# Kernel optimization log

Measured on AMD Instinct MI355X. Metric: run time of the kernel, lower is better.

Reference implementation:

```python
import jax, jax.numpy as jnp
import numpy as np

N_STREAMS = 4
TAU = 1.0
ALPHA = 0.1
CAYLEY_ITERS = 2
LN_EPS = 1e-5


def setup_inputs() -> dict:
    key = jax.random.key(0)
    k1, k2, k3 = jax.random.split(key, 3)
    b, l, d = 2, 4096, 2048
    n = N_STREAMS
    x = jax.random.normal(k1, (b, l, d), dtype=jnp.float32)
    ln_w = jnp.ones((d,), dtype=jnp.float32)
    ln_b = jnp.zeros((d,), dtype=jnp.float32)
    # CastedLinear: trunc_normal std = 1/sqrt(in_features)
    proj_w = jax.random.truncated_normal(k2, -2.0, 2.0, (3 * n * n, d), dtype=jnp.float32) / jnp.sqrt(d * 1.0)
    proj_b = jnp.zeros((3 * n * n,), dtype=jnp.float32)
    # sublayer_fn realized as a dense linear (typical transformer sublayer core)
    W_sub = jax.random.normal(k3, (d, d), dtype=jnp.float32) / jnp.sqrt(d * 1.0)
    return {"x": x, "ln_w": ln_w, "ln_b": ln_b, "proj_w": proj_w, "proj_b": proj_b, "W_sub": W_sub}


def _layernorm(x, w, b):
    mu = jnp.mean(x, axis=-1, keepdims=True)
    var = jnp.mean(jnp.square(x - mu), axis=-1, keepdims=True)
    return (x - mu) * jax.lax.rsqrt(var + LN_EPS) * w + b


def _iterative_cayley(raw):
    # raw: (b, l, n, n) fp32
    w = raw - jnp.swapaxes(raw, -1, -2)
    eye = jnp.eye(N_STREAMS, dtype=raw.dtype)
    y = eye + ALPHA * w
    for _ in range(CAYLEY_ITERS):
        y = eye + 0.5 * ALPHA * jnp.matmul(w, eye + y)
    return y


def reference(x, ln_w, ln_b, proj_w, proj_b, W_sub):
    b, l, d = x.shape
    n = N_STREAMS
    gates = _layernorm(x, ln_w, ln_b) @ proj_w.T + proj_b  # (b, l, 3*n*n)
    pre_raw, post_raw, res_raw = jnp.split(gates, 3, axis=-1)
    pre_raw = pre_raw.reshape(b, l, n, n).astype(jnp.float32)
    post_raw = post_raw.reshape(b, l, n, n).astype(jnp.float32)
    res_raw = res_raw.reshape(b, l, n, n).astype(jnp.float32)
    h_pre = jax.nn.softmax(pre_raw / TAU, axis=-1)
    h_post = jax.nn.softmax(post_raw / TAU, axis=-2)
    h_res = _iterative_cayley(res_raw)
    # All streams of x_streams are identical copies of x, so
    # einsum('blij,bljd->blid', h, x_streams).mean(-2) == mean_i(sum_j h[i,j]) * x.
    coeff_pre = jnp.mean(jnp.sum(h_pre, axis=-1), axis=-1)    # (b, l)
    coeff_res = jnp.mean(jnp.sum(h_res, axis=-1), axis=-1)    # (b, l)
    coeff_post = jnp.mean(jnp.sum(h_post, axis=-1), axis=-1)  # (b, l)
    x_in = coeff_pre[..., None] * x
    y = x_in @ W_sub  # sublayer_fn
    return coeff_res[..., None] * x + coeff_post[..., None] * y
```

## Files before the change

### kernel.cpp

```cpp
#include <hip/hip_runtime.h>
#include <stdint.h>


typedef __attribute__((ext_vector_type(8))) __bf16 bf16x8;
typedef __attribute__((ext_vector_type(4))) float f32x4;
typedef __attribute__((ext_vector_type(8))) unsigned short us8;
typedef __attribute__((ext_vector_type(4))) unsigned short us4;

__device__ __forceinline__ unsigned short f2bf(float f) {
  union { float f; unsigned int u; } v; v.f = f;
  unsigned int u = v.u;
  u += 0x7fffu + ((u >> 16) & 1u);
  return (unsigned short)(u >> 16);
}

__device__ __forceinline__ void gload_lds16(const void* g, void* l) {
  __builtin_amdgcn_global_load_lds(
      (__attribute__((address_space(1))) void*)g,
      (__attribute__((address_space(3))) void*)l, 16, 0, 0);
}

__global__ __launch_bounds__(256) void k_ln_conv(
    const float* __restrict__ x, const float* __restrict__ lw, const float* __restrict__ lb,
    unsigned short* __restrict__ xb, unsigned short* __restrict__ lnb, int D) {
  const int t = blockIdx.x;
  const int tid = threadIdx.x;
  const float* row = x + (size_t)t * D;
  f32x4 a = *(const f32x4*)(row + tid * 8);
  f32x4 b = *(const f32x4*)(row + tid * 8 + 4);
  float vv[8] = {a[0], a[1], a[2], a[3], b[0], b[1], b[2], b[3]};
  float s = 0.f, ss = 0.f;
#pragma unroll
  for (int j = 0; j < 8; ++j) { s += vv[j]; ss += vv[j] * vv[j]; }
#pragma unroll
  for (int off = 32; off > 0; off >>= 1) { s += __shfl_down(s, off); ss += __shfl_down(ss, off); }
  __shared__ float red[8];
  __shared__ float st[2];
  int lane = tid & 63, wv = tid >> 6;
  if (lane == 0) { red[wv] = s; red[4 + wv] = ss; }
  __syncthreads();
  if (tid == 0) {
    float S = red[0] + red[1] + red[2] + red[3];
    float SS = red[4] + red[5] + red[6] + red[7];
    float mu = S / (float)D;
    float var = SS / (float)D - mu * mu;
    st[0] = mu; st[1] = rsqrtf(var + 1e-5f);
  }
  __syncthreads();
  float mu = st[0], rstd = st[1];
  f32x4 w0 = *(const f32x4*)(lw + tid * 8), w1 = *(const f32x4*)(lw + tid * 8 + 4);
  f32x4 b0 = *(const f32x4*)(lb + tid * 8), b1 = *(const f32x4*)(lb + tid * 8 + 4);
  float ww[8] = {w0[0], w0[1], w0[2], w0[3], w1[0], w1[1], w1[2], w1[3]};
  float bb[8] = {b0[0], b0[1], b0[2], b0[3], b1[0], b1[1], b1[2], b1[3]};
  us8 ox, ol;
#pragma unroll
  for (int j = 0; j < 8; ++j) {
    ox[j] = f2bf(vv[j]);
    ol[j] = f2bf((vv[j] - mu) * rstd * ww[j] + bb[j]);
  }
  *(us8*)(xb + (size_t)t * D + tid * 8) = ox;
  *(us8*)(lnb + (size_t)t * D + tid * 8) = ol;
}

__global__ __launch_bounds__(256) void k_wt(const float* __restrict__ W,
                                            unsigned short* __restrict__ Wt, int D) {
  __shared__ float tile[64][65];
  int kb = blockIdx.x * 64, nb = blockIdx.y * 64;
  int tid = threadIdx.x;
  int tx = tid & 15, ty = tid >> 4;
#pragma unroll
  for (int p = 0; p < 4; ++p) {
    int r = p * 16 + ty;
    f32x4 v = *(const f32x4*)(W + (size_t)(kb + r) * D + nb + tx * 4);
    tile[r][tx * 4 + 0] = v[0]; tile[r][tx * 4 + 1] = v[1];
    tile[r][tx * 4 + 2] = v[2]; tile[r][tx * 4 + 3] = v[3];
  }
  __syncthreads();
#pragma unroll
  for (int p = 0; p < 2; ++p) {
    int c = p * 256 + tid;
    int nr = c >> 3, kc = (c & 7) * 8;
    us8 o;
#pragma unroll
    for (int j = 0; j < 8; ++j) o[j] = f2bf(tile[kc + j][nr]);
    *(us8*)(Wt + (size_t)(nb + nr) * D + kb + kc) = o;
  }
}

__global__ void k_pconv(const float* __restrict__ p, unsigned short* __restrict__ q, int n) {
  int i = (blockIdx.x * 256 + threadIdx.x) * 4;
  if (i < n) {
    f32x4 v = *(const f32x4*)(p + i);
    us4 o;
#pragma unroll
    for (int j = 0; j < 4; ++j) o[j] = f2bf(v[j]);
    *(us4*)(q + i) = o;
  }
}

__global__ __launch_bounds__(256) void k_gates(
    const unsigned short* __restrict__ A,
    const unsigned short* __restrict__ Bp,
    const float* __restrict__ pb,
    float* __restrict__ cresp, float* __restrict__ cpyp, int K) {
  __shared__ __attribute__((aligned(16))) unsigned short As[128 * 32];
  __shared__ __attribute__((aligned(16))) unsigned short Bs[48 * 32];
  __shared__ float gl[128][49];
  __shared__ float pbs[48];
  int tid = threadIdx.x, lane = tid & 63, wv = tid >> 6;
  if (tid < 48) pbs[tid] = pb[tid];
  f32x4 acc[2][3] = {};
  size_t rowBase = (size_t)blockIdx.x * 128;
  for (int k0 = 0; k0 < K; k0 += 32) {
#pragma unroll
    for (int inst = 0; inst < 2; ++inst) {
      int eo = inst * 2048 + wv * 512 + lane * 8;
      int r = eo >> 5, cc = eo & 31;
      gload_lds16(A + (rowBase + r) * K + k0 + cc, (char*)As + inst * 4096 + wv * 1024);
    }
    if (tid < 192) {
      int r = tid >> 2, cc = (tid & 3) * 8;
      us8 v = *(const us8*)(Bp + (size_t)r * K + k0 + cc);
      *(us8*)(Bs + r * 32 + cc) = v;
    }
    __syncthreads();
    int kb = (lane >> 4) * 8, rr = lane & 15;
    bf16x8 av[2], bv[3];
#pragma unroll
    for (int mi = 0; mi < 2; ++mi)
      av[mi] = *(const bf16x8*)(As + (wv * 32 + mi * 16 + rr) * 32 + kb);
#pragma unroll
    for (int ni = 0; ni < 3; ++ni)
      bv[ni] = *(const bf16x8*)(Bs + (ni * 16 + rr) * 32 + kb);
#pragma unroll
    for (int mi = 0; mi < 2; ++mi)
#pragma unroll
      for (int ni = 0; ni < 3; ++ni)
        acc[mi][ni] = __builtin_amdgcn_mfma_f32_16x16x32_bf16(av[mi], bv[ni], acc[mi][ni], 0, 0, 0);
    __syncthreads();
  }
#pragma unroll
  for (int mi = 0; mi < 2; ++mi)
#pragma unroll
    for (int ni = 0; ni < 3; ++ni)
#pragma unroll
      for (int i = 0; i < 4; ++i)
        gl[wv * 32 + mi * 16 + (lane >> 4) * 4 + i][ni * 16 + (lane & 15)] = acc[mi][ni][i];
  __syncthreads();
  if (tid < 128) {
    float g[48];
#pragma unroll
    for (int j = 0; j < 48; ++j) g[j] = gl[tid][j] + pbs[j];
    float cpre = 0.f;
#pragma unroll
    for (int i = 0; i < 4; ++i) {
      float m = fmaxf(fmaxf(g[i * 4], g[i * 4 + 1]), fmaxf(g[i * 4 + 2], g[i * 4 + 3]));
      float e0 = expf(g[i * 4] - m), e1 = expf(g[i * 4 + 1] - m);
      float e2 = expf(g[i * 4 + 2] - m), e3 = expf(g[i * 4 + 3] - m);
      float inv = 1.f / (e0 + e1 + e2 + e3);
      cpre += e0 * inv + e1 * inv + e2 * inv + e3 * inv;
    }
    cpre *= 0.25f;
    float cpost = 0.f;
#pragma unroll
    for (int j = 0; j < 4; ++j) {
      float a0 = g[16 + j], a1 = g[20 + j], a2 = g[24 + j], a3 = g[28 + j];
      float m = fmaxf(fmaxf(a0, a1), fmaxf(a2, a3));
      float e0 = expf(a0 - m), e1 = expf(a1 - m), e2 = expf(a2 - m), e3 = expf(a3 - m);
      float inv = 1.f / (e0 + e1 + e2 + e3);
      cpost += e0 * inv + e1 * inv + e2 * inv + e3 * inv;
    }
    cpost *= 0.25f;
    float w4[16], y4[16];
#pragma unroll
    for (int i = 0; i < 4; ++i)
#pragma unroll
      for (int j = 0; j < 4; ++j)
        w4[i * 4 + j] = g[32 + i * 4 + j] - g[32 + j * 4 + i];
#pragma unroll
    for (int i = 0; i < 16; ++i) y4[i] = 0.1f * w4[i];
    y4[0] += 1.f; y4[5] += 1.f; y4[10] += 1.f; y4[15] += 1.f;
#pragma unroll
    for (int it = 0; it < 2; ++it) {
      float z[16];
#pragma unroll
      for (int i = 0; i < 16; ++i) z[i] = y4[i];
      z[0] += 1.f; z[5] += 1.f; z[10] += 1.f; z[15] += 1.f;
#pragma unroll
      for (int i = 0; i < 4; ++i)
#pragma unroll
        for (int j = 0; j < 4; ++j) {
          float acc2 = 0.f;
#pragma unroll
          for (int k = 0; k < 4; ++k) acc2 += w4[i * 4 + k] * z[k * 4 + j];
          y4[i * 4 + j] = ((i == j) ? 1.f : 0.f) + 0.05f * acc2;
        }
    }
    float cr = 0.f;
#pragma unroll
    for (int i = 0; i < 16; ++i) cr += y4[i];
    cr *= 0.25f;
    cresp[rowBase + tid] = cr;
    cpyp[rowBase + tid] = cpre * cpost;
  }
}

__global__ __launch_bounds__(512, 2) void k_gemm(
    const unsigned short* __restrict__ A,
    const unsigned short* __restrict__ Bt,
    const float* __restrict__ x,
    const float* __restrict__ cresp, const float* __restrict__ cpyp,
    float* __restrict__ out, int M, int N, int K) {
  __shared__ __attribute__((aligned(16))) unsigned short As[4][256 * 32];
  __shared__ __attribute__((aligned(16))) unsigned short Bs[4][256 * 32];
  const int tid = threadIdx.x, lane = tid & 63, wv = tid >> 6;
  const int nbn = N >> 8;
  const int nwg = (M >> 8) * nbn;
  const int chunk = nwg >> 3;
  const int gid = (blockIdx.x & 7) * chunk + (blockIdx.x >> 3);
  const int bm = gid / nbn, bn = gid % nbn;
  const int wm = wv >> 2, wn = wv & 3;
  const int rr = lane & 15, ksl = lane >> 4;
  const int koff = (ksl ^ ((rr >> 1) & 3)) * 8;
  const int rloc = tid >> 2;
  const int cbelem = ((tid & 3) ^ ((tid >> 3) & 3)) * 8;
  const unsigned short* aG = A + (size_t)((bm << 8) + rloc) * K + cbelem;
  const unsigned short* bG = Bt + (size_t)((bn << 8) + rloc) * K + cbelem;
  f32x4 acc[8][4] = {};
  const int nsl = K >> 5;

#define STAGE(KT, SLOT)                                                        \
  {                                                                            \
    const unsigned short* ag_ = aG + (KT) * 32;                                \
    const unsigned short* bg_ = bG + (KT) * 32;                                \
    unsigned short* la_ = &As[(SLOT)][wv * 512];                               \
    unsigned short* lb_ = &Bs[(SLOT)][wv * 512];                               \
    gload_lds16(ag_, la_);                                                     \
    gload_lds16(ag_ + (size_t)128 * K, la_ + 4096);                            \
    gload_lds16(bg_, lb_);                                                     \
    gload_lds16(bg_ + (size_t)128 * K, lb_ + 4096);                            \
  }

  STAGE(0, 0)
  STAGE(1, 1)
  STAGE(2, 2)

#define GBODY(S)                                                               \
  {                                                                            \
    asm volatile("s_waitcnt vmcnt(8)" ::: "memory");                           \
    __builtin_amdgcn_sched_barrier(0);                                         \
    __builtin_amdgcn_s_barrier();                                              \
    __builtin_amdgcn_sched_barrier(0);                                         \
    int kt_ = jb + (S) + 3;                                                    \
    if (kt_ > nsl - 1) kt_ = nsl - 1;                                          \
    STAGE(kt_, ((S) + 3) & 3)                                                  \
    __builtin_amdgcn_sched_barrier(0);                                         \
    const unsigned short* Ab = &As[(S)][(wm * 128 + rr) * 32 + koff];          \
    const unsigned short* Bb = &Bs[(S)][(wn * 64 + rr) * 32 + koff];           \
    bf16x8 av[8], bv[4];                                                       \
    _Pragma("unroll")                                                          \
    for (int mf = 0; mf < 8; ++mf) av[mf] = *(const bf16x8*)(Ab + mf * 512);   \
    _Pragma("unroll")                                                          \
    for (int nf = 0; nf < 4; ++nf) bv[nf] = *(const bf16x8*)(Bb + nf * 512);   \
    __builtin_amdgcn_s_setprio(1);                                             \
    _Pragma("unroll")                                                          \
    for (int mf = 0; mf < 8; ++mf)                                             \
      _Pragma("unroll")                                                        \
      for (int nf = 0; nf < 4; ++nf)                                           \
        acc[mf][nf] =                                                          \
            __builtin_amdgcn_mfma_f32_16x16x32_bf16(av[mf], bv[nf],            \
                                                    acc[mf][nf], 0, 0, 0);     \
    __builtin_amdgcn_s_setprio(0);                                             \
  }

  for (int jb = 0; jb < nsl; jb += 4) {
    GBODY(0)
    GBODY(1)
    GBODY(2)
    GBODY(3)
  }
#undef GBODY
#undef STAGE

  const int orow0 = (bm << 8) + wm * 128 + ksl * 4;
  const int ocol0 = (bn << 8) + wn * 64 + rr;
#pragma unroll
  for (int mf = 0; mf < 8; ++mf)
#pragma unroll
    for (int i = 0; i < 4; ++i) {
      const int row = orow0 + mf * 16 + i;
      const float crv = cresp[row], cpv = cpyp[row];
      const size_t base = (size_t)row * N + ocol0;
#pragma unroll
      for (int nf = 0; nf < 4; ++nf)
        out[base + nf * 16] = crv * x[base + nf * 16] + cpv * acc[mf][nf][i];
    }
}

extern "C" void kernel_launch(void* const* d_in, const int* in_sizes, int n_in,
                              void* d_out, int out_size, void* d_ws, size_t ws_size,
                              hipStream_t stream) {
  const float* x  = (const float*)d_in[0];
  const float* lw = (const float*)d_in[1];
  const float* lb = (const float*)d_in[2];
  const float* pw = (const float*)d_in[3];
  const float* pb = (const float*)d_in[4];
  const float* W  = (const float*)d_in[5];
  float* out = (float*)d_out;

  const int D = in_sizes[1];
  const int M = in_sizes[0] / D;
  const int G = in_sizes[4];

  char* ws = (char*)d_ws;
  size_t off = 0;
  unsigned short* xb  = (unsigned short*)(ws + off); off += (size_t)M * D * 2;
  unsigned short* lnb = (unsigned short*)(ws + off); off += (size_t)M * D * 2;
  unsigned short* Wt  = (unsigned short*)(ws + off); off += (size_t)D * D * 2;
  unsigned short* pjb = (unsigned short*)(ws + off); off += (size_t)G * D * 2;
  float* cres = (float*)(ws + off); off += (size_t)M * 4;
  float* cpy  = (float*)(ws + off); off += (size_t)M * 4;

  k_ln_conv<<<M, 256, 0, stream>>>(x, lw, lb, xb, lnb, D);
  k_wt<<<dim3(D / 64, D / 64), 256, 0, stream>>>(W, Wt, D);
  k_pconv<<<(G * D / 4 + 255) / 256, 256, 0, stream>>>(pw, pjb, G * D);
  k_gates<<<M / 128, 256, 0, stream>>>(lnb, pjb, pb, cres, cpy, D);

  const int nwg = (M / 256) * (D / 256);
  k_gemm<<<nwg, 512, 0, stream>>>(xb, Wt, x, cres, cpy, out, M, D, D);
}
```

Measured before the change: 139.7 us.

## Prefetch next K-slice B fragments into registers while computing current slice

Restructures the GEMM main loop so B fragments for the next K-slice are loaded from LDS into a ping-pong register buffer during the current slice's MFMA block, with a prologue loading the first slice. The wait count is tightened to vmcnt(4) so the next LDS slot is resident before it is read. This aims to hide LDS read latency behind MFMAs, at the cost of extra VGPRs and a tighter wait on the global-to-LDS pipeline.

```diff
diff --git a/kernel.cpp b/kernel.cpp
--- a/kernel.cpp
+++ b/kernel.cpp
@@ -241,13 +241,9 @@
     gload_lds16(bg_ + (size_t)128 * K, lb_ + 4096);                            \
   }
 
-  STAGE(0, 0)
-  STAGE(1, 1)
-  STAGE(2, 2)
-
-#define GBODY(S)                                                               \
+#define REGION(S, BVC, BVN)                                                    \
   {                                                                            \
-    asm volatile("s_waitcnt vmcnt(8)" ::: "memory");                           \
+    asm volatile("s_waitcnt vmcnt(4)" ::: "memory");                           \
     __builtin_amdgcn_sched_barrier(0);                                         \
     __builtin_amdgcn_s_barrier();                                              \
     __builtin_amdgcn_sched_barrier(0);                                         \
@@ -255,31 +251,42 @@
     if (kt_ > nsl - 1) kt_ = nsl - 1;                                          \
     STAGE(kt_, ((S) + 3) & 3)                                                  \
     __builtin_amdgcn_sched_barrier(0);                                         \
-    const unsigned short* Ab = &As[(S)][(wm * 128 + rr) * 32 + koff];          \
-    const unsigned short* Bb = &Bs[(S)][(wn * 64 + rr) * 32 + koff];           \
-    bf16x8 av[8], bv[4];                                                       \
+    const unsigned short* Ab = &As[(S) & 3][(wm * 128 + rr) * 32 + koff];      \
+    bf16x8 av[8];                                                              \
     _Pragma("unroll")                                                          \
     for (int mf = 0; mf < 8; ++mf) av[mf] = *(const bf16x8*)(Ab + mf * 512);   \
+    const unsigned short* Bb = &Bs[((S) + 1) & 3][(wn * 64 + rr) * 32 + koff]; \
     _Pragma("unroll")                                                          \
-    for (int nf = 0; nf < 4; ++nf) bv[nf] = *(const bf16x8*)(Bb + nf * 512);   \
+    for (int nf = 0; nf < 4; ++nf) BVN[nf] = *(const bf16x8*)(Bb + nf * 512);  \
     __builtin_amdgcn_s_setprio(1);                                             \
     _Pragma("unroll")                                                          \
     for (int mf = 0; mf < 8; ++mf)                                             \
       _Pragma("unroll")                                                        \
       for (int nf = 0; nf < 4; ++nf)                                           \
-        acc[mf][nf] =                                                          \
-            __builtin_amdgcn_mfma_f32_16x16x32_bf16(av[mf], bv[nf],            \
-                                                    acc[mf][nf], 0, 0, 0);     \
+        acc[mf][nf] = __builtin_amdgcn_mfma_f32_16x16x32_bf16(                 \
+            av[mf], BVC[nf], acc[mf][nf], 0, 0, 0);                            \
     __builtin_amdgcn_s_setprio(0);                                             \
   }
 
+  bf16x8 bvP[4], bvQ[4];
+  STAGE(0, 0)
+  STAGE(1, 1)
+  STAGE(2, 2)
+  asm volatile("s_waitcnt vmcnt(8)" ::: "memory");
+  __builtin_amdgcn_sched_barrier(0);
+  __builtin_amdgcn_s_barrier();
+  {
+    const unsigned short* Bb = &Bs[0][(wn * 64 + rr) * 32 + koff];
+#pragma unroll
+    for (int nf = 0; nf < 4; ++nf) bvP[nf] = *(const bf16x8*)(Bb + nf * 512);
+  }
   for (int jb = 0; jb < nsl; jb += 4) {
-    GBODY(0)
-    GBODY(1)
-    GBODY(2)
-    GBODY(3)
-  }
-#undef GBODY
+    REGION(0, bvP, bvQ)
+    REGION(1, bvQ, bvP)
+    REGION(2, bvP, bvQ)
+    REGION(3, bvQ, bvP)
+  }
+#undef REGION
 #undef STAGE
 
   const int orow0 = (bm << 8) + wm * 128 + ksl * 4;
```

Result: slower. 143.5 us (+2.7%).
